# Optimization experiments

Hardware: AMD Instinct MI355X
Metric: run time of the kernel (lower is better)

Reference implementation:

```python
import jax, jax.numpy as jnp
import numpy as np

V = 32000   # vocab_size
T = 2048    # train_len (pos embed table size)
E = 1024    # embed_dim
H = 16      # num_heads
FF = 4096   # ff_dim
L = 4       # num_layers
B, C = 2, 1024
D = E // H  # head_dim = 64
EPS = 1e-5


def setup_inputs() -> dict:
    key = jax.random.key(0)
    ks = jax.random.split(key, 12)
    s = 0.02
    inp = {
        "x": jax.random.randint(ks[0], (B, C), 0, V),
        "embed": jax.random.normal(ks[1], (V, E), jnp.float32) * s,
        "pos_embed": jax.random.normal(ks[2], (T, E), jnp.float32) * s,
        "Wq": jax.random.normal(ks[3], (L, E, E), jnp.float32) * s,
        "Wk": jax.random.normal(ks[4], (L, E, E), jnp.float32) * s,
        "Wv": jax.random.normal(ks[5], (L, E, E), jnp.float32) * s,
        "Wo": jax.random.normal(ks[6], (L, E, E), jnp.float32) * s,
        "ln1_w": jnp.ones((L, E), jnp.float32),
        "ln1_b": jnp.zeros((L, E), jnp.float32),
        "ln2_w": jnp.ones((L, E), jnp.float32),
        "ln2_b": jnp.zeros((L, E), jnp.float32),
        "W1": jax.random.normal(ks[7], (L, E, FF), jnp.float32) * s,
        "b1": jnp.zeros((L, FF), jnp.float32),
        "W2": jax.random.normal(ks[8], (L, FF, E), jnp.float32) * s,
        "b2": jnp.zeros((L, E), jnp.float32),
        "lnf_w": jnp.ones((E,), jnp.float32),
        "lnf_b": jnp.zeros((E,), jnp.float32),
        "Wout": jax.random.normal(ks[9], (E, V), jnp.float32) * s,
        "bout": jnp.zeros((V,), jnp.float32),
    }
    return inp


def _layernorm(h, w, b):
    mu = jnp.mean(h, axis=-1, keepdims=True)
    var = jnp.var(h, axis=-1, keepdims=True)
    return (h - mu) * jax.lax.rsqrt(var + EPS) * w + b


def reference(x, embed, pos_embed, Wq, Wk, Wv, Wo, ln1_w, ln1_b, ln2_w, ln2_b,
              W1, b1, W2, b2, lnf_w, lnf_b, Wout, bout):
    Bx, Cx = x.shape
    positions = jnp.clip(jnp.arange(Cx), 0, T - 1)  # 'clamp' extrapolation
    h = embed[x] + pos_embed[positions]             # [B,C,E]
    # causal mask: -inf above the diagonal
    mask = jnp.where(jnp.tril(jnp.ones((Cx, Cx), bool)), 0.0, -jnp.inf).astype(h.dtype)
    scale = 1.0 / np.sqrt(D)
    for i in range(L):
        hn = _layernorm(h, ln1_w[i], ln1_b[i])
        Q = (hn @ Wq[i]).reshape(Bx, Cx, H, D).transpose(0, 2, 1, 3)  # [B,H,C,D]
        K = (hn @ Wk[i]).reshape(Bx, Cx, H, D).transpose(0, 2, 1, 3)
        Vv = (hn @ Wv[i]).reshape(Bx, Cx, H, D).transpose(0, 2, 1, 3)
        scores = jnp.einsum('bhqd,bhkd->bhqk', Q, K) * scale + mask
        weights = jax.nn.softmax(scores, axis=-1)
        attn = jnp.einsum('bhqk,bhkd->bhqd', weights, Vv)
        attn = attn.transpose(0, 2, 1, 3).reshape(Bx, Cx, E) @ Wo[i]
        h = h + attn
        hn2 = _layernorm(h, ln2_w[i], ln2_b[i])
        h = h + jax.nn.gelu(hn2 @ W1[i] + b1[i], approximate=False) @ W2[i] + b2[i]
    return _layernorm(h, lnf_w, lnf_b) @ Wout + bout  # [B,C,V]
```

## Files before the change

kernel.cpp:

```cpp
#include <hip/hip_runtime.h>
#include <hip/hip_bf16.h>
#include <math.h>

constexpr int V  = 32000;
constexpr int E  = 1024;
constexpr int H  = 16;
constexpr int FF = 4096;
constexpr int L  = 4;
constexpr int B  = 2;
constexpr int C  = 1024;
constexpr int D  = 64;
constexpr int N  = B * C;
constexpr int E3 = 3 * E;
constexpr float EPS = 1e-5f;

typedef __hip_bfloat16 bf16;
typedef __bf16 bf16x8 __attribute__((ext_vector_type(8)));
typedef __bf16 bf16x4 __attribute__((ext_vector_type(4)));
typedef float  f32x4  __attribute__((ext_vector_type(4)));

#define AS1 __attribute__((address_space(1)))
#define AS3 __attribute__((address_space(3)))

__device__ inline bf16x8 lds_load8(const bf16* p) {
    bf16x4 lo = *(const bf16x4*)p;
    bf16x4 hi = *(const bf16x4*)(p + 4);
    bf16x8 r;
    r[0]=lo[0]; r[1]=lo[1]; r[2]=lo[2]; r[3]=lo[3];
    r[4]=hi[0]; r[5]=hi[1]; r[6]=hi[2]; r[7]=hi[3];
    return r;
}
__device__ inline void lds_store8(bf16* p, bf16x8 v) {
    bf16x4 lo, hi;
    lo[0]=v[0]; lo[1]=v[1]; lo[2]=v[2]; lo[3]=v[3];
    hi[0]=v[4]; hi[1]=v[5]; hi[2]=v[6]; hi[3]=v[7];
    *(bf16x4*)p = lo; *(bf16x4*)(p + 4) = hi;
}

__device__ inline bf16x8 lds_frag32(const bf16* sbase, int row, int c) {
    return *(const bf16x8*)(sbase + row * 32 + ((c ^ ((row >> 1) & 3)) << 3));
}
__device__ inline bf16x8 lds_frag64(const bf16* sbase, int row, int c) {
    return *(const bf16x8*)(sbase + row * 64 + ((c ^ (row & 7)) << 3));
}

__global__ void embed_kernel(const int* __restrict__ x,
                             const float* __restrict__ embed,
                             const float* __restrict__ pos,
                             float* __restrict__ h) {
    int token = blockIdx.x;
    int c = token % C;
    int id = x[token];
    const float* erow = embed + (size_t)id * E;
    const float* prow = pos   + (size_t)c  * E;
    float* hrow = h + (size_t)token * E;
    for (int e = threadIdx.x; e < E; e += blockDim.x)
        hrow[e] = erow[e] + prow[e];
}

__global__ void layernorm_kernel(const float* __restrict__ in,
                                 const float* __restrict__ w,
                                 const float* __restrict__ b,
                                 bf16* __restrict__ out) {
    __shared__ float red[256];
    int token = blockIdx.x;
    int tid = threadIdx.x;
    float4 xv = ((const float4*)(in + (size_t)token * E))[tid];

    red[tid] = xv.x + xv.y + xv.z + xv.w;
    __syncthreads();
    for (int st = 128; st > 0; st >>= 1) {
        if (tid < st) red[tid] += red[tid + st];
        __syncthreads();
    }
    float mu = red[0] * (1.0f / E);
    __syncthreads();

    float d0 = xv.x - mu, d1 = xv.y - mu, d2 = xv.z - mu, d3 = xv.w - mu;
    red[tid] = d0 * d0 + d1 * d1 + d2 * d2 + d3 * d3;
    __syncthreads();
    for (int st = 128; st > 0; st >>= 1) {
        if (tid < st) red[tid] += red[tid + st];
        __syncthreads();
    }
    float var = red[0] * (1.0f / E);
    float inv = rsqrtf(var + EPS);

    float4 wv = ((const float4*)w)[tid];
    float4 bv = ((const float4*)b)[tid];
    float y0 = d0 * inv * wv.x + bv.x;
    float y1 = d1 * inv * wv.y + bv.y;
    float y2 = d2 * inv * wv.z + bv.z;
    float y3 = d3 * inv * wv.w + bv.w;
    ushort4 o;
    { bf16 t0 = __float2bfloat16(y0); o.x = *(ushort*)&t0; }
    { bf16 t1 = __float2bfloat16(y1); o.y = *(ushort*)&t1; }
    { bf16 t2 = __float2bfloat16(y2); o.z = *(ushort*)&t2; }
    { bf16 t3 = __float2bfloat16(y3); o.w = *(ushort*)&t3; }
    ((ushort4*)(out + (size_t)token * E))[tid] = o;
}

__global__ void transpose_all(const float* __restrict__ Wq,
                              const float* __restrict__ Wk,
                              const float* __restrict__ Wv,
                              const float* __restrict__ Wo,
                              const float* __restrict__ W1,
                              const float* __restrict__ W2,
                              const float* __restrict__ Wout,
                              bf16* __restrict__ qkvt, bf16* __restrict__ wot,
                              bf16* __restrict__ w1t,  bf16* __restrict__ w2t,
                              bf16* __restrict__ wvt) {
    __shared__ float tile[64][65];
    int b = blockIdx.x;
    const float* src; bf16* dst;
    int Nn, Kk, n0, k0;
    if (b >= 12288) {
        int rem = b - 12288;
        src = Wout; dst = wvt; Nn = V; Kk = E;
        n0 = (rem % 500) * 64; k0 = (rem / 500) * 64;
    } else {
        int i = b / 3072, r = b % 3072;
        if (r < 1024) {
            int mat = r >> 8, rr = r & 255;
            n0 = (rr & 15) * 64; k0 = (rr >> 4) * 64;
            Nn = E; Kk = E;
            const float* srcs[4] = {Wq, Wk, Wv, Wo};
            src = srcs[mat] + (size_t)i * E * E;
            dst = (mat < 3) ? qkvt + ((size_t)i * E3 + (size_t)mat * E) * E
                            : wot + (size_t)i * E * E;
        } else if (r < 2048) {
            int rr = r - 1024;
            n0 = (rr & 63) * 64; k0 = (rr >> 6) * 64;
            Nn = FF; Kk = E;
            src = W1 + (size_t)i * E * FF;
            dst = w1t + (size_t)i * FF * E;
        } else {
            int rr = r - 2048;
            n0 = (rr & 15) * 64; k0 = (rr >> 4) * 64;
            Nn = E; Kk = FF;
            src = W2 + (size_t)i * FF * E;
            dst = w2t + (size_t)i * E * FF;
        }
    }
    int tid = threadIdx.x;
    #pragma unroll
    for (int it = 0; it < 4; ++it) {
        int idx = it * 256 + tid;
        int row = idx >> 4, c4 = (idx & 15) * 4;
        *(float4*)&tile[row][c4] =
            *(const float4*)&src[(size_t)(k0 + row) * Nn + n0 + c4];
    }
    __syncthreads();
    #pragma unroll
    for (int it = 0; it < 2; ++it) {
        int s = it * 256 + tid;
        int nrow = s >> 3, kc = s & 7;
        bf16x8 v;
        #pragma unroll
        for (int j = 0; j < 8; ++j)
            v[j] = (__bf16)__float2bfloat16(tile[kc * 8 + j][nrow]);
        *(bf16x8*)&dst[(size_t)(n0 + nrow) * Kk + k0 + kc * 8] = v;
    }
}

__global__ void transpose_v(const bf16* __restrict__ qkv,
                            bf16* __restrict__ vt) {
    __shared__ ushort tile[32][34];
    int c0 = blockIdx.x * 32;
    int d0 = (blockIdx.y & 1) * 32;
    int bh = blockIdx.y >> 1;
    int bb = bh >> 4, hh = bh & 15;
    int tx = threadIdx.x & 31, ty = threadIdx.x >> 5;
    const ushort* src = (const ushort*)qkv;
    ushort* dst = (ushort*)vt;
    #pragma unroll
    for (int i = 0; i < 32; i += 8)
        tile[ty + i][tx] = src[(size_t)(bb * C + c0 + ty + i) * E3 + 2 * E + hh * D + d0 + tx];
    __syncthreads();
    #pragma unroll
    for (int i = 0; i < 32; i += 8)
        dst[((size_t)bh * D + d0 + ty + i) * C + c0 + tx] = tile[tx][ty + i];
}

__launch_bounds__(512, 2)
__global__ void gemm_v8(const bf16* __restrict__ A,
                        const bf16* __restrict__ Bt,
                        const float* __restrict__ bias,
                        float* __restrict__ outF,
                        int M, int Nc, int K) {
    __shared__ __align__(16) bf16 sA[2][2][128 * 64];
    __shared__ __align__(16) bf16 sB[2][2][128 * 64];

    int tid  = threadIdx.x;
    int lane = tid & 63;
    int wid  = tid >> 6;
    int wm   = wid >> 2;
    int wn   = wid & 3;
    int l16  = lane & 15;
    int lhi  = lane >> 4;

    int nwg = gridDim.x * gridDim.y;
    int id  = blockIdx.y * gridDim.x + blockIdx.x;
    int cpx = nwg >> 3;
    int swz = (id & 7) * cpx + (id >> 3);
    int bx  = swz / gridDim.y;
    int by  = swz % gridDim.y;

    size_t brow = (size_t)by * 256;
    size_t bcol = (size_t)bx * 256;

    f32x4 acc[8][4] = {};

    auto stageA = [&](int buf, int half, int t) {
        size_t k0 = (size_t)t * 64;
        #pragma unroll
        for (int j = 0; j < 2; ++j) {
            int s = j * 512 + tid;
            int row = s >> 3;
            int ch  = (s & 7) ^ (row & 7);
            int ldso = (j * 512 + wid * 64) * 8;
            const bf16* g = A + (brow + half * 128 + row) * K + k0 + ch * 8;
            __builtin_amdgcn_global_load_lds(
                (const AS1 void*)g, (AS3 void*)(&sA[buf][half][0] + ldso), 16, 0, 0);
        }
    };
    auto stageB = [&](int buf, int half, int t) {
        size_t k0 = (size_t)t * 64;
        #pragma unroll
        for (int j = 0; j < 2; ++j) {
            int s = j * 512 + tid;
            int row = s >> 3;
            int ch  = (s & 7) ^ (row & 7);
            int ldso = (j * 512 + wid * 64) * 8;
            const bf16* g = Bt + (bcol + half * 128 + row) * K + k0 + ch * 8;
            __builtin_amdgcn_global_load_lds(
                (const AS1 void*)g, (AS3 void*)(&sB[buf][half][0] + ldso), 16, 0, 0);
        }
    };

    int NT = K / 64;
    stageA(0, 0, 0); stageB(0, 0, 0);
    stageB(0, 1, 0); stageA(0, 1, 0);
    stageA(1, 0, 1); stageB(1, 0, 1);

    bf16x8 ra[4][2], rb[2][2], rb0[2][2];

    for (int t = 0; t < NT; ++t) {
        int cur = t & 1, nxt = cur ^ 1;

        if (t == NT - 1) asm volatile("s_waitcnt vmcnt(4)" ::: "memory");
        else             asm volatile("s_waitcnt vmcnt(8)" ::: "memory");
        __builtin_amdgcn_sched_barrier(0);
        __builtin_amdgcn_s_barrier();
        if (t + 1 < NT) { stageB(nxt, 1, t + 1); stageA(nxt, 1, t + 1); }
        #pragma unroll
        for (int m = 0; m < 4; ++m)
            #pragma unroll
            for (int kh = 0; kh < 2; ++kh)
                ra[m][kh] = lds_frag64(&sA[cur][0][0], wm * 64 + m * 16 + l16, kh * 4 + lhi);
        #pragma unroll
        for (int n = 0; n < 2; ++n)
            #pragma unroll
            for (int kh = 0; kh < 2; ++kh)
                rb0[n][kh] = lds_frag64(&sB[cur][0][0], wn * 32 + n * 16 + l16, kh * 4 + lhi);
        __builtin_amdgcn_s_setprio(1);
        #pragma unroll
        for (int m = 0; m < 4; ++m)
            #pragma unroll
            for (int n = 0; n < 2; ++n)
                #pragma unroll
                for (int kh = 0; kh < 2; ++kh)
                    acc[m][n] = __builtin_amdgcn_mfma_f32_16x16x32_bf16(
                        ra[m][kh], rb0[n][kh], acc[m][n], 0, 0, 0);
        __builtin_amdgcn_s_setprio(0);

        if (t == NT - 1) asm volatile("s_waitcnt vmcnt(0)" ::: "memory");
        else             asm volatile("s_waitcnt vmcnt(8)" ::: "memory");
        __builtin_amdgcn_sched_barrier(0);
        __builtin_amdgcn_s_barrier();
        #pragma unroll
        for (int n = 0; n < 2; ++n)
            #pragma unroll
            for (int kh = 0; kh < 2; ++kh)
                rb[n][kh] = lds_frag64(&sB[cur][1][0], wn * 32 + n * 16 + l16, kh * 4 + lhi);
        __builtin_amdgcn_s_setprio(1);
        #pragma unroll
        for (int m = 0; m < 4; ++m)
            #pragma unroll
            for (int n = 0; n < 2; ++n)
                #pragma unroll
                for (int kh = 0; kh < 2; ++kh)
                    acc[m][n + 2] = __builtin_amdgcn_mfma_f32_16x16x32_bf16(
                        ra[m][kh], rb[n][kh], acc[m][n + 2], 0, 0, 0);
        __builtin_amdgcn_s_setprio(0);

        if (t + 2 < NT) { stageA(cur, 0, t + 2); stageB(cur, 0, t + 2); }
        #pragma unroll
        for (int m = 0; m < 4; ++m)
            #pragma unroll
            for (int kh = 0; kh < 2; ++kh)
                ra[m][kh] = lds_frag64(&sA[cur][1][0], wm * 64 + m * 16 + l16, kh * 4 + lhi);
        __builtin_amdgcn_s_setprio(1);
        #pragma unroll
        for (int m = 0; m < 4; ++m)
            #pragma unroll
            for (int n = 0; n < 2; ++n)
                #pragma unroll
                for (int kh = 0; kh < 2; ++kh)
                    acc[m + 4][n + 2] = __builtin_amdgcn_mfma_f32_16x16x32_bf16(
                        ra[m][kh], rb[n][kh], acc[m + 4][n + 2], 0, 0, 0);
        __builtin_amdgcn_s_setprio(0);

        __builtin_amdgcn_s_setprio(1);
        #pragma unroll
        for (int m = 0; m < 4; ++m)
            #pragma unroll
            for (int n = 0; n < 2; ++n)
                #pragma unroll
                for (int kh = 0; kh < 2; ++kh)
                    acc[m + 4][n] = __builtin_amdgcn_mfma_f32_16x16x32_bf16(
                        ra[m][kh], rb0[n][kh], acc[m + 4][n], 0, 0, 0);
        __builtin_amdgcn_s_setprio(0);
    }

    int crow = lhi * 4;
    #pragma unroll
    for (int qm = 0; qm < 2; ++qm)
        #pragma unroll
        for (int qn = 0; qn < 2; ++qn)
            #pragma unroll
            for (int m = 0; m < 4; ++m)
                #pragma unroll
                for (int n = 0; n < 2; ++n)
                    #pragma unroll
                    for (int r = 0; r < 4; ++r) {
                        size_t row = brow + qm * 128 + wm * 64 + m * 16 + crow + r;
                        size_t col = bcol + qn * 128 + wn * 32 + n * 16 + l16;
                        float val = acc[qm * 4 + m][qn * 2 + n][r];
                        val += bias[col];
                        outF[row * Nc + col] = val;
                    }
}

__launch_bounds__(256, 2)
__global__ void gemm_bf16_128(const bf16* __restrict__ A,
                              const bf16* __restrict__ Bt,
                              const float* __restrict__ bias,
                              const float* __restrict__ res,
                              float* __restrict__ outF,
                              bf16*  __restrict__ outB,
                              int M, int Nc, int K, int gelu_flag) {
    __shared__ __align__(16) bf16 sA[4][128 * 32];
    __shared__ __align__(16) bf16 sB[4][128 * 32];

    int tid  = threadIdx.x;
    int lane = tid & 63;
    int wid  = tid >> 6;
    int wr   = wid >> 1;
    int wc   = wid & 1;
    int l16  = lane & 15;
    int lhi  = lane >> 4;

    int nwg = gridDim.x * gridDim.y;
    int id  = blockIdx.y * gridDim.x + blockIdx.x;
    int cpx = nwg >> 3;
    int swz = (id & 7) * cpx + (id >> 3);
    int bx  = swz / gridDim.y;
    int by  = swz % gridDim.y;

    size_t brow = (size_t)by * 128;
    size_t bcol = (size_t)bx * 128;

    f32x4 acc[4][4] = {};

    auto stage = [&](int buf, int t) {
        size_t k0 = (size_t)t * 32;
        #pragma unroll
        for (int j = 0; j < 2; ++j) {
            int s = j * 256 + tid;
            int row = s >> 2;
            int ch  = (s & 3) ^ ((row >> 1) & 3);
            int ldso = (j * 256 + wid * 64) * 8;
            const bf16* ga = A + (brow + row) * K + k0 + ch * 8;
            __builtin_amdgcn_global_load_lds(
                (const AS1 void*)ga, (AS3 void*)(&sA[buf][0] + ldso), 16, 0, 0);
        }
        #pragma unroll
        for (int j = 0; j < 2; ++j) {
            int s = j * 256 + tid;
            int row = s >> 2;
            int ch  = (s & 3) ^ ((row >> 1) & 3);
            int ldso = (j * 256 + wid * 64) * 8;
            const bf16* gb = Bt + (bcol + row) * K + k0 + ch * 8;
            __builtin_amdgcn_global_load_lds(
                (const AS1 void*)gb, (AS3 void*)(&sB[buf][0] + ldso), 16, 0, 0);
        }
    };

    int NT = K / 32;
    stage(0, 0);
    stage(1, 1);

    for (int t = 0; t < NT; ++t) {
        if (t + 2 < NT) {
            stage((t + 2) & 3, t + 2);
            asm volatile("s_waitcnt vmcnt(8)" ::: "memory");
        } else if (t + 1 < NT) {
            asm volatile("s_waitcnt vmcnt(4)" ::: "memory");
        } else {
            asm volatile("s_waitcnt vmcnt(0)" ::: "memory");
        }
        __builtin_amdgcn_sched_barrier(0);
        __builtin_amdgcn_s_barrier();

        const bf16* As_ = &sA[t & 3][0];
        const bf16* Bs_ = &sB[t & 3][0];
        bf16x8 ra[4], rb[4];
        #pragma unroll
        for (int m = 0; m < 4; ++m)
            ra[m] = lds_frag32(As_, wr * 64 + m * 16 + l16, lhi);
        #pragma unroll
        for (int n = 0; n < 4; ++n)
            rb[n] = lds_frag32(Bs_, wc * 64 + n * 16 + l16, lhi);

        __builtin_amdgcn_s_setprio(1);
        #pragma unroll
        for (int m = 0; m < 4; ++m)
            #pragma unroll
            for (int n = 0; n < 4; ++n)
                acc[m][n] = __builtin_amdgcn_mfma_f32_16x16x32_bf16(
                    ra[m], rb[n], acc[m][n], 0, 0, 0);
        __builtin_amdgcn_s_setprio(0);
    }

    int crow = lhi * 4;
    #pragma unroll
    for (int m = 0; m < 4; ++m) {
        #pragma unroll
        for (int n = 0; n < 4; ++n) {
            #pragma unroll
            for (int r = 0; r < 4; ++r) {
                size_t row = brow + wr * 64 + m * 16 + crow + r;
                size_t col = bcol + wc * 64 + n * 16 + l16;
                float val = acc[m][n][r];
                if (bias) val += bias[col];
                if (gelu_flag) val = 0.5f * val * (1.0f + erff(val * 0.70710678118f));
                if (res) val += res[row * Nc + col];
                if (outF) outF[row * Nc + col] = val;
                if (outB) outB[row * Nc + col] = __float2bfloat16(val);
            }
        }
    }
}

__launch_bounds__(256, 3)
__global__ void gemm_bf16_64(const bf16* __restrict__ A,
                             const bf16* __restrict__ Bt,
                             const float* __restrict__ bias,
                             const float* __restrict__ res,
                             float* __restrict__ outF,
                             bf16*  __restrict__ outB,
                             int M, int Nc, int K, int gelu_flag) {
    __shared__ __align__(16) bf16 sA[4][64 * 32];
    __shared__ __align__(16) bf16 sB[4][128 * 32];

    int tid  = threadIdx.x;
    int lane = tid & 63;
    int wid  = tid >> 6;
    int l16  = lane & 15;
    int lhi  = lane >> 4;

    int nwg = gridDim.x * gridDim.y;
    int id  = blockIdx.y * gridDim.x + blockIdx.x;
    int cpx = nwg >> 3;
    int swz = (id & 7) * cpx + (id >> 3);
    int bx  = swz / gridDim.y;
    int by  = swz % gridDim.y;

    size_t brow = (size_t)by * 64;
    size_t bcol = (size_t)bx * 128;

    f32x4 acc[4][2] = {};

    auto stage = [&](int buf, int t) {
        size_t k0 = (size_t)t * 32;
        {
            int s = tid;
            int row = s >> 2;
            int ch  = (s & 3) ^ ((row >> 1) & 3);
            int ldso = (wid * 64) * 8;
            const bf16* ga = A + (brow + row) * K + k0 + ch * 8;
            __builtin_amdgcn_global_load_lds(
                (const AS1 void*)ga, (AS3 void*)(&sA[buf][0] + ldso), 16, 0, 0);
        }
        #pragma unroll
        for (int j = 0; j < 2; ++j) {
            int s = j * 256 + tid;
            int row = s >> 2;
            int ch  = (s & 3) ^ ((row >> 1) & 3);
            int ldso = (j * 256 + wid * 64) * 8;
            const bf16* gb = Bt + (bcol + row) * K + k0 + ch * 8;
            __builtin_amdgcn_global_load_lds(
                (const AS1 void*)gb, (AS3 void*)(&sB[buf][0] + ldso), 16, 0, 0);
        }
    };

    int NT = K / 32;
    stage(0, 0);
    stage(1, 1);

    for (int t = 0; t < NT; ++t) {
        if (t + 2 < NT) {
            stage((t + 2) & 3, t + 2);
            asm volatile("s_waitcnt vmcnt(6)" ::: "memory");
        } else if (t + 1 < NT) {
            asm volatile("s_waitcnt vmcnt(3)" ::: "memory");
        } else {
            asm volatile("s_waitcnt vmcnt(0)" ::: "memory");
        }
        __builtin_amdgcn_sched_barrier(0);
        __builtin_amdgcn_s_barrier();

        const bf16* As_ = &sA[t & 3][0];
        const bf16* Bs_ = &sB[t & 3][0];
        bf16x8 ra[4], rb[2];
        #pragma unroll
        for (int m = 0; m < 4; ++m)
            ra[m] = lds_frag32(As_, m * 16 + l16, lhi);
        #pragma unroll
        for (int n = 0; n < 2; ++n)
            rb[n] = lds_frag32(Bs_, wid * 32 + n * 16 + l16, lhi);

        __builtin_amdgcn_s_setprio(1);
        #pragma unroll
        for (int m = 0; m < 4; ++m)
            #pragma unroll
            for (int n = 0; n < 2; ++n)
                acc[m][n] = __builtin_amdgcn_mfma_f32_16x16x32_bf16(
                    ra[m], rb[n], acc[m][n], 0, 0, 0);
        __builtin_amdgcn_s_setprio(0);
    }

    int crow = lhi * 4;
    #pragma unroll
    for (int m = 0; m < 4; ++m) {
        #pragma unroll
        for (int n = 0; n < 2; ++n) {
            #pragma unroll
            for (int r = 0; r < 4; ++r) {
                size_t row = brow + m * 16 + crow + r;
                size_t col = bcol + wid * 32 + n * 16 + l16;
                float val = acc[m][n][r];
                if (bias) val += bias[col];
                if (gelu_flag) val = 0.5f * val * (1.0f + erff(val * 0.70710678118f));
                if (res) val += res[row * Nc + col];
                if (outF) outF[row * Nc + col] = val;
                if (outB) outB[row * Nc + col] = __float2bfloat16(val);
            }
        }
    }
}

constexpr int QBLK = 128;
constexpr int KVB  = 64;
constexpr int PSTR = 72;

__launch_bounds__(512)
__global__ void flash_attn(const bf16* __restrict__ qkv,
                           const bf16* __restrict__ vt,
                           bf16* __restrict__ O) {
    __shared__ bf16 sK[KVB][PSTR];
    __shared__ bf16 sV[D][PSTR];
    __shared__ bf16 sP[8][16][PSTR];

    int qt = blockIdx.x;
    int bh = blockIdx.y;
    int bb = bh >> 4, hh = bh & 15;
    int qbase = qt * QBLK;
    int tid = threadIdx.x, lane = tid & 63, w = tid >> 6;
    int l16 = lane & 15, lhi = lane >> 4;

    int qrow = qbase + w * 16 + l16;
    const bf16* qp = qkv + (size_t)(bb * C + qrow) * E3 + hh * D + lhi * 8;
    bf16x8 qf0 = *(const bf16x8*)qp;
    bf16x8 qf1 = *(const bf16x8*)(qp + 32);

    f32x4 oa[4] = {};
    float m_run[4] = {-INFINITY, -INFINITY, -INFINITY, -INFINITY};
    float l_run[4] = {0.f, 0.f, 0.f, 0.f};

    int NTk = 2 * qt + 2;
    for (int t = 0; t < NTk; ++t) {
        int k0 = t * KVB;
        {
            int row = tid >> 3, c8 = tid & 7;
            bf16x8 kv = *(const bf16x8*)(qkv + (size_t)(bb * C + k0 + row) * E3 + E + hh * D + c8 * 8);
            lds_store8(&sK[row][c8 * 8], kv);
            bf16x8 vv = *(const bf16x8*)(vt + ((size_t)bh * D + row) * C + k0 + c8 * 8);
            lds_store8(&sV[row][c8 * 8], vv);
        }
        __syncthreads();

        f32x4 sc[4] = {};
        #pragma unroll
        for (int n = 0; n < 4; ++n) {
            bf16x8 kf0 = lds_load8(&sK[n * 16 + l16][lhi * 8]);
            sc[n] = __builtin_amdgcn_mfma_f32_16x16x32_bf16(qf0, kf0, sc[n], 0, 0, 0);
            bf16x8 kf1 = lds_load8(&sK[n * 16 + l16][32 + lhi * 8]);
            sc[n] = __builtin_amdgcn_mfma_f32_16x16x32_bf16(qf1, kf1, sc[n], 0, 0, 0);
        }

        int qg = qbase + w * 16 + lhi * 4;
        #pragma unroll
        for (int n = 0; n < 4; ++n) {
            int kg = k0 + n * 16 + l16;
            #pragma unroll
            for (int r = 0; r < 4; ++r) {
                float vvv = sc[n][r] * 0.125f;
                if (t >= 2 * qt && kg > qg + r) vvv = -1e30f;
                sc[n][r] = vvv;
            }
        }

        float pm[4];
        #pragma unroll
        for (int r = 0; r < 4; ++r)
            pm[r] = fmaxf(fmaxf(sc[0][r], sc[1][r]), fmaxf(sc[2][r], sc[3][r]));
        #pragma unroll
        for (int xm = 1; xm <= 8; xm <<= 1)
            #pragma unroll
            for (int r = 0; r < 4; ++r)
                pm[r] = fmaxf(pm[r], __shfl_xor(pm[r], xm));

        float corr[4];
        #pragma unroll
        for (int r = 0; r < 4; ++r) {
            float mn = fmaxf(m_run[r], pm[r]);
            corr[r] = __expf(m_run[r] - mn);
            m_run[r] = mn;
        }
        f32x4 p[4];
        #pragma unroll
        for (int n = 0; n < 4; ++n)
            #pragma unroll
            for (int r = 0; r < 4; ++r)
                p[n][r] = __expf(sc[n][r] - m_run[r]);

        float rsum[4];
        #pragma unroll
        for (int r = 0; r < 4; ++r)
            rsum[r] = p[0][r] + p[1][r] + p[2][r] + p[3][r];
        #pragma unroll
        for (int xm = 1; xm <= 8; xm <<= 1)
            #pragma unroll
            for (int r = 0; r < 4; ++r)
                rsum[r] += __shfl_xor(rsum[r], xm);
        #pragma unroll
        for (int r = 0; r < 4; ++r)
            l_run[r] = l_run[r] * corr[r] + rsum[r];
        #pragma unroll
        for (int nd = 0; nd < 4; ++nd)
            #pragma unroll
            for (int r = 0; r < 4; ++r)
                oa[nd][r] *= corr[r];

        #pragma unroll
        for (int n = 0; n < 4; ++n)
            #pragma unroll
            for (int r = 0; r < 4; ++r)
                sP[w][lhi * 4 + r][n * 16 + l16] = __float2bfloat16(p[n][r]);
        bf16x8 pa0 = lds_load8(&sP[w][l16][lhi * 8]);
        bf16x8 pa1 = lds_load8(&sP[w][l16][32 + lhi * 8]);

        #pragma unroll
        for (int nd = 0; nd < 4; ++nd) {
            bf16x8 vf0 = lds_load8(&sV[nd * 16 + l16][lhi * 8]);
            oa[nd] = __builtin_amdgcn_mfma_f32_16x16x32_bf16(pa0, vf0, oa[nd], 0, 0, 0);
            bf16x8 vf1 = lds_load8(&sV[nd * 16 + l16][32 + lhi * 8]);
            oa[nd] = __builtin_amdgcn_mfma_f32_16x16x32_bf16(pa1, vf1, oa[nd], 0, 0, 0);
        }
        __syncthreads();
    }

    #pragma unroll
    for (int r = 0; r < 4; ++r) {
        float inv = 1.0f / l_run[r];
        int qg = qbase + w * 16 + lhi * 4 + r;
        bf16* orow = O + (size_t)(bb * C + qg) * E + hh * D;
        #pragma unroll
        for (int nd = 0; nd < 4; ++nd)
            orow[nd * 16 + l16] = __float2bfloat16(oa[nd][r] * inv);
    }
}

extern "C" void kernel_launch(void* const* d_in, const int* in_sizes, int n_in,
                              void* d_out, int out_size, void* d_ws, size_t ws_size,
                              hipStream_t stream) {
    const int*   x     = (const int*)  d_in[0];
    const float* embed = (const float*)d_in[1];
    const float* pos   = (const float*)d_in[2];
    const float* Wq    = (const float*)d_in[3];
    const float* Wk    = (const float*)d_in[4];
    const float* Wv    = (const float*)d_in[5];
    const float* Wo    = (const float*)d_in[6];
    const float* ln1w  = (const float*)d_in[7];
    const float* ln1b  = (const float*)d_in[8];
    const float* ln2w  = (const float*)d_in[9];
    const float* ln2b  = (const float*)d_in[10];
    const float* W1    = (const float*)d_in[11];
    const float* b1    = (const float*)d_in[12];
    const float* W2    = (const float*)d_in[13];
    const float* b2    = (const float*)d_in[14];
    const float* lnfw  = (const float*)d_in[15];
    const float* lnfb  = (const float*)d_in[16];
    const float* Wout  = (const float*)d_in[17];
    const float* bout  = (const float*)d_in[18];
    float* out = (float*)d_out;

    char* p = (char*)d_ws;
    auto alloc = [&](size_t bytes) {
        char* r = p;
        p += (bytes + 255) & ~(size_t)255;
        return r;
    };
    float* h    = (float*)alloc((size_t)N * E  * 4);
    bf16*  qkvb = (bf16*) alloc((size_t)N * E3 * 2);
    bf16*  hn   = (bf16*) alloc((size_t)N * E  * 2);
    bf16*  attn = (bf16*) alloc((size_t)N * E  * 2);
    bf16*  ff   = (bf16*) alloc((size_t)N * FF * 2);
    bf16*  vt   = (bf16*) alloc((size_t)B * H * D * C * 2);
    bf16*  qkvt = (bf16*) alloc((size_t)L * E3 * E * 2);
    bf16*  wot  = (bf16*) alloc((size_t)L * E  * E * 2);
    bf16*  w1t  = (bf16*) alloc((size_t)L * FF * E * 2);
    bf16*  w2t  = (bf16*) alloc((size_t)L * E  * FF * 2);
    bf16*  wvt  = (bf16*) alloc((size_t)V * E  * 2 + 4096);

    transpose_all<<<20288, 256, 0, stream>>>(Wq, Wk, Wv, Wo, W1, W2, Wout,
                                             qkvt, wot, w1t, w2t, wvt);

    embed_kernel<<<N, 256, 0, stream>>>(x, embed, pos, h);

    dim3 gQKV(E3 / 128, N / 128);
    dim3 gF  (FF / 128, N / 128);
    dim3 gV  (V  / 256, N / 256);
    dim3 gO  (E  / 128, N / 64);

    for (int i = 0; i < L; ++i) {
        layernorm_kernel<<<N, 256, 0, stream>>>(h, ln1w + i * E, ln1b + i * E, hn);

        gemm_bf16_128<<<gQKV, 256, 0, stream>>>(hn, qkvt + (size_t)i * E3 * E,
                                                nullptr, nullptr, nullptr, qkvb,
                                                N, E3, E, 0);

        transpose_v<<<dim3(C / 32, 2 * B * H), 256, 0, stream>>>(qkvb, vt);

        flash_attn<<<dim3(C / QBLK, B * H), 512, 0, stream>>>(qkvb, vt, attn);

        gemm_bf16_64<<<gO, 256, 0, stream>>>(attn, wot + (size_t)i * E * E,
                                             nullptr, h, h, nullptr,
                                             N, E, E, 0);

        layernorm_kernel<<<N, 256, 0, stream>>>(h, ln2w + i * E, ln2b + i * E, hn);

        gemm_bf16_128<<<gF, 256, 0, stream>>>(hn, w1t + (size_t)i * FF * E,
                                              b1 + (size_t)i * FF, nullptr,
                                              nullptr, ff,
                                              N, FF, E, 1);
        gemm_bf16_64<<<gO, 256, 0, stream>>>(ff, w2t + (size_t)i * E * FF,
                                             b2 + (size_t)i * E, h, h, nullptr,
                                             N, E, FF, 0);
    }

    layernorm_kernel<<<N, 256, 0, stream>>>(h, lnfw, lnfb, hn);
    gemm_v8<<<gV, 512, 0, stream>>>(hn, wvt, bout, out, N, V, E);
}
```

Measured before the change: 1.239 ms.

## Fuse embed with first layernorm, deepen gemm_bf16_64 K-tile, retile flash attention

Merges the embedding add with the first layer's layernorm so one launch and one full read of h are dropped. gemm_bf16_64 moves from four 32-wide K stages to three 64-wide stages with a 64-column swizzle, which halves the barrier count per K. Its occupancy hint drops from 3 to 2 blocks to fit the larger LDS buffers. flash_attn goes to 64-row query blocks with 256 threads, reverses tile order on odd heads to balance causal work, and register-prefetches the next K/V tile while the current one is consumed.

```diff
diff --git a/kernel.cpp b/kernel.cpp
--- a/kernel.cpp
+++ b/kernel.cpp
@@ -44,18 +44,56 @@
     return *(const bf16x8*)(sbase + row * 64 + ((c ^ (row & 7)) << 3));
 }
 
-__global__ void embed_kernel(const int* __restrict__ x,
-                             const float* __restrict__ embed,
-                             const float* __restrict__ pos,
-                             float* __restrict__ h) {
+__global__ void embed_ln_kernel(const int* __restrict__ x,
+                                const float* __restrict__ embed,
+                                const float* __restrict__ pos,
+                                const float* __restrict__ w,
+                                const float* __restrict__ b,
+                                float* __restrict__ h,
+                                bf16* __restrict__ hn) {
+    __shared__ float red[256];
     int token = blockIdx.x;
+    int tid = threadIdx.x;
     int c = token % C;
     int id = x[token];
-    const float* erow = embed + (size_t)id * E;
-    const float* prow = pos   + (size_t)c  * E;
-    float* hrow = h + (size_t)token * E;
-    for (int e = threadIdx.x; e < E; e += blockDim.x)
-        hrow[e] = erow[e] + prow[e];
+    float4 ev = ((const float4*)(embed + (size_t)id * E))[tid];
+    float4 pv = ((const float4*)(pos + (size_t)c * E))[tid];
+    float4 xv;
+    xv.x = ev.x + pv.x; xv.y = ev.y + pv.y;
+    xv.z = ev.z + pv.z; xv.w = ev.w + pv.w;
+    ((float4*)(h + (size_t)token * E))[tid] = xv;
+
+    red[tid] = xv.x + xv.y + xv.z + xv.w;
+    __syncthreads();
+    for (int st = 128; st > 0; st >>= 1) {
+        if (tid < st) red[tid] += red[tid + st];
+        __syncthreads();
+    }
+    float mu = red[0] * (1.0f / E);
+    __syncthreads();
+
+    float d0 = xv.x - mu, d1 = xv.y - mu, d2 = xv.z - mu, d3 = xv.w - mu;
+    red[tid] = d0 * d0 + d1 * d1 + d2 * d2 + d3 * d3;
+    __syncthreads();
+    for (int st = 128; st > 0; st >>= 1) {
+        if (tid < st) red[tid] += red[tid + st];
+        __syncthreads();
+    }
+    float var = red[0] * (1.0f / E);
+    float inv = rsqrtf(var + EPS);
+
+    float4 wv = ((const float4*)w)[tid];
+    float4 bv = ((const float4*)b)[tid];
+    float y0 = d0 * inv * wv.x + bv.x;
+    float y1 = d1 * inv * wv.y + bv.y;
+    float y2 = d2 * inv * wv.z + bv.z;
+    float y3 = d3 * inv * wv.w + bv.w;
+    ushort4 o;
+    { bf16 t0 = __float2bfloat16(y0); o.x = *(ushort*)&t0; }
+    { bf16 t1 = __float2bfloat16(y1); o.y = *(ushort*)&t1; }
+    { bf16 t2 = __float2bfloat16(y2); o.z = *(ushort*)&t2; }
+    { bf16 t3 = __float2bfloat16(y3); o.w = *(ushort*)&t3; }
+    ((ushort4*)(hn + (size_t)token * E))[tid] = o;
 }
 
 __global__ void layernorm_kernel(const float* __restrict__ in,
@@ -453,7 +491,7 @@
     }
 }
 
-__launch_bounds__(256, 3)
+__launch_bounds__(256, 2)
 __global__ void gemm_bf16_64(const bf16* __restrict__ A,
                              const bf16* __restrict__ Bt,
                              const float* __restrict__ bias,
@@ -461,8 +499,8 @@
                              float* __restrict__ outF,
                              bf16*  __restrict__ outB,
                              int M, int Nc, int K, int gelu_flag) {
-    __shared__ __align__(16) bf16 sA[4][64 * 32];
-    __shared__ __align__(16) bf16 sB[4][128 * 32];
+    __shared__ __align__(16) bf16 sA[3][64 * 64];
+    __shared__ __align__(16) bf16 sB[3][128 * 64];
 
     int tid  = threadIdx.x;
     int lane = tid & 63;
@@ -483,21 +521,22 @@
     f32x4 acc[4][2] = {};
 
     auto stage = [&](int buf, int t) {
-        size_t k0 = (size_t)t * 32;
-        {
-            int s = tid;
-            int row = s >> 2;
-            int ch  = (s & 3) ^ ((row >> 1) & 3);
-            int ldso = (wid * 64) * 8;
+        size_t k0 = (size_t)t * 64;
+        #pragma unroll
+        for (int j = 0; j < 2; ++j) {
+            int s = j * 256 + tid;
+            int row = s >> 3;
+            int ch  = (s & 7) ^ (row & 7);
+            int ldso = (j * 256 + wid * 64) * 8;
             const bf16* ga = A + (brow + row) * K + k0 + ch * 8;
             __builtin_amdgcn_global_load_lds(
                 (const AS1 void*)ga, (AS3 void*)(&sA[buf][0] + ldso), 16, 0, 0);
         }
         #pragma unroll
-        for (int j = 0; j < 2; ++j) {
+        for (int j = 0; j < 4; ++j) {
             int s = j * 256 + tid;
-            int row = s >> 2;
-            int ch  = (s & 3) ^ ((row >> 1) & 3);
+            int row = s >> 3;
+            int ch  = (s & 7) ^ (row & 7);
             int ldso = (j * 256 + wid * 64) * 8;
             const bf16* gb = Bt + (bcol + row) * K + k0 + ch * 8;
             __builtin_amdgcn_global_load_lds(
@@ -505,40 +544,44 @@
         }
     };
 
-    int NT = K / 32;
-    stage(0, 0);
-    stage(1, 1);
+    int NT = K / 64;
+    stage(0, 0); stage(1, 1);
+    int cur = 0, sl2 = 2;
 
     for (int t = 0; t < NT; ++t) {
-        if (t + 2 < NT) {
-            stage((t + 2) & 3, t + 2);
-            asm volatile("s_waitcnt vmcnt(6)" ::: "memory");
-        } else if (t + 1 < NT) {
-            asm volatile("s_waitcnt vmcnt(3)" ::: "memory");
-        } else {
-            asm volatile("s_waitcnt vmcnt(0)" ::: "memory");
-        }
+        if (t == NT - 1) asm volatile("s_waitcnt vmcnt(0)" ::: "memory");
+        else             asm volatile("s_waitcnt vmcnt(6)" ::: "memory");
         __builtin_amdgcn_sched_barrier(0);
         __builtin_amdgcn_s_barrier();
-
-        const bf16* As_ = &sA[t & 3][0];
-        const bf16* Bs_ = &sB[t & 3][0];
-        bf16x8 ra[4], rb[2];
-        #pragma unroll
-        for (int m = 0; m < 4; ++m)
-            ra[m] = lds_frag32(As_, m * 16 + l16, lhi);
+        if (t + 2 < NT) stage(sl2, t + 2);
+
+        const bf16* As_ = &sA[cur][0];
+        const bf16* Bs_ = &sB[cur][0];
+        bf16x8 ra[4][2], rb[2][2];
+        #pragma unroll
+        for (int m = 0; m < 4; ++m)
+            #pragma unroll
+            for (int kh = 0; kh < 2; ++kh)
+                ra[m][kh] = lds_frag64(As_, m * 16 + l16, kh * 4 + lhi);
         #pragma unroll
         for (int n = 0; n < 2; ++n)
-            rb[n] = lds_frag32(Bs_, wid * 32 + n * 16 + l16, lhi);
+            #pragma unroll
+            for (int kh = 0; kh < 2; ++kh)
+                rb[n][kh] = lds_frag64(Bs_, wid * 32 + n * 16 + l16, kh * 4 + lhi);
 
         __builtin_amdgcn_s_setprio(1);
         #pragma unroll
         for (int m = 0; m < 4; ++m)
             #pragma unroll
             for (int n = 0; n < 2; ++n)
-                acc[m][n] = __builtin_amdgcn_mfma_f32_16x16x32_bf16(
-                    ra[m], rb[n], acc[m][n], 0, 0, 0);
+                #pragma unroll
+                for (int kh = 0; kh < 2; ++kh)
+                    acc[m][n] = __builtin_amdgcn_mfma_f32_16x16x32_bf16(
+                        ra[m][kh], rb[n][kh], acc[m][n], 0, 0, 0);
         __builtin_amdgcn_s_setprio(0);
+
+        cur = (cur == 2) ? 0 : cur + 1;
+        sl2 = (sl2 == 2) ? 0 : sl2 + 1;
     }
 
     int crow = lhi * 4;
@@ -561,20 +604,21 @@
     }
 }
 
-constexpr int QBLK = 128;
+constexpr int QBLK = 64;
 constexpr int KVB  = 64;
 constexpr int PSTR = 72;
 
-__launch_bounds__(512)
+__launch_bounds__(256)
 __global__ void flash_attn(const bf16* __restrict__ qkv,
                            const bf16* __restrict__ vt,
                            bf16* __restrict__ O) {
     __shared__ bf16 sK[KVB][PSTR];
     __shared__ bf16 sV[D][PSTR];
-    __shared__ bf16 sP[8][16][PSTR];
+    __shared__ bf16 sP[4][16][PSTR];
 
     int qt = blockIdx.x;
     int bh = blockIdx.y;
+    if (bh & 1) qt = (C / QBLK - 1) - qt;
     int bb = bh >> 4, hh = bh & 15;
     int qbase = qt * QBLK;
     int tid = threadIdx.x, lane = tid & 63, w = tid >> 6;
@@ -589,18 +633,34 @@
     float m_run[4] = {-INFINITY, -INFINITY, -INFINITY, -INFINITY};
     float l_run[4] = {0.f, 0.f, 0.f, 0.f};
 
-    int NTk = 2 * qt + 2;
+    int NTk = qt + 1;
+    int srow = tid >> 3, sc8 = tid & 7;
+    int srow2 = srow + 32;
+
+    bf16x8 kvR0, kvR1, vvR0, vvR1;
+    kvR0 = *(const bf16x8*)(qkv + (size_t)(bb * C + srow)  * E3 + E + hh * D + sc8 * 8);
+    kvR1 = *(const bf16x8*)(qkv + (size_t)(bb * C + srow2) * E3 + E + hh * D + sc8 * 8);
+    vvR0 = *(const bf16x8*)(vt + ((size_t)bh * D + srow)  * C + sc8 * 8);
+    vvR1 = *(const bf16x8*)(vt + ((size_t)bh * D + srow2) * C + sc8 * 8);
+
     for (int t = 0; t < NTk; ++t) {
+        __syncthreads();
+        lds_store8(&sK[srow][sc8 * 8],  kvR0);
+        lds_store8(&sK[srow2][sc8 * 8], kvR1);
+        lds_store8(&sV[srow][sc8 * 8],  vvR0);
+        lds_store8(&sV[srow2][sc8 * 8], vvR1);
+
+        bf16x8 kvN0, kvN1, vvN0, vvN1;
+        if (t + 1 < NTk) {
+            int k0n = (t + 1) * KVB;
+            kvN0 = *(const bf16x8*)(qkv + (size_t)(bb * C + k0n + srow)  * E3 + E + hh * D + sc8 * 8);
+            kvN1 = *(const bf16x8*)(qkv + (size_t)(bb * C + k0n + srow2) * E3 + E + hh * D + sc8 * 8);
+            vvN0 = *(const bf16x8*)(vt + ((size_t)bh * D + srow)  * C + k0n + sc8 * 8);
+            vvN1 = *(const bf16x8*)(vt + ((size_t)bh * D + srow2) * C + k0n + sc8 * 8);
+        }
+        __syncthreads();
+
         int k0 = t * KVB;
-        {
-            int row = tid >> 3, c8 = tid & 7;
-            bf16x8 kv = *(const bf16x8*)(qkv + (size_t)(bb * C + k0 + row) * E3 + E + hh * D + c8 * 8);
-            lds_store8(&sK[row][c8 * 8], kv);
-            bf16x8 vv = *(const bf16x8*)(vt + ((size_t)bh * D + row) * C + k0 + c8 * 8);
-            lds_store8(&sV[row][c8 * 8], vv);
-        }
-        __syncthreads();
-
         f32x4 sc[4] = {};
         #pragma unroll
         for (int n = 0; n < 4; ++n) {
@@ -617,7 +677,7 @@
             #pragma unroll
             for (int r = 0; r < 4; ++r) {
                 float vvv = sc[n][r] * 0.125f;
-                if (t >= 2 * qt && kg > qg + r) vvv = -1e30f;
+                if (t == qt && kg > qg + r) vvv = -1e30f;
                 sc[n][r] = vvv;
             }
         }
@@ -679,7 +739,8 @@
             bf16x8 vf1 = lds_load8(&sV[nd * 16 + l16][32 + lhi * 8]);
             oa[nd] = __builtin_amdgcn_mfma_f32_16x16x32_bf16(pa1, vf1, oa[nd], 0, 0, 0);
         }
-        __syncthreads();
+
+        if (t + 1 < NTk) { kvR0 = kvN0; kvR1 = kvN1; vvR0 = vvN0; vvR1 = vvN1; }
     }
 
     #pragma unroll
@@ -738,7 +799,7 @@
     transpose_all<<<20288, 256, 0, stream>>>(Wq, Wk, Wv, Wo, W1, W2, Wout,
                                              qkvt, wot, w1t, w2t, wvt);
 
-    embed_kernel<<<N, 256, 0, stream>>>(x, embed, pos, h);
+    embed_ln_kernel<<<N, 256, 0, stream>>>(x, embed, pos, ln1w, ln1b, h, hn);
 
     dim3 gQKV(E3 / 128, N / 128);
     dim3 gF  (FF / 128, N / 128);
@@ -746,7 +807,8 @@
     dim3 gO  (E  / 128, N / 64);
 
     for (int i = 0; i < L; ++i) {
-        layernorm_kernel<<<N, 256, 0, stream>>>(h, ln1w + i * E, ln1b + i * E, hn);
+        if (i > 0)
+            layernorm_kernel<<<N, 256, 0, stream>>>(h, ln1w + i * E, ln1b + i * E, hn);
 
         gemm_bf16_128<<<gQKV, 256, 0, stream>>>(hn, qkvt + (size_t)i * E3 * E,
                                                 nullptr, nullptr, nullptr, qkvb,
@@ -754,7 +816,7 @@
 
         transpose_v<<<dim3(C / 32, 2 * B * H), 256, 0, stream>>>(qkvb, vt);
 
-        flash_attn<<<dim3(C / QBLK, B * H), 512, 0, stream>>>(qkvb, vt, attn);
+        flash_attn<<<dim3(C / QBLK, B * H), 256, 0, stream>>>(qkvb, vt, attn);
 
         gemm_bf16_64<<<gO, 256, 0, stream>>>(attn, wot + (size_t)i * E * E,
                                              nullptr, h, h, nullptr,
```

After: 1.223 ms (median of 2 runs). No clear change (-1.3%).
